# Kernel optimization log

Hardware: AMD Instinct MI355X
Metric: run time of the kernel (lower is better)

The kernel has to match this reference:

```python
import jax, jax.numpy as jnp
import numpy as np

VOCAB, EMB, UNITS, B, T = 50000, 300, 256, 32, 512


def _lstm_scan(x, Wi, Wh, b, h0, c0):
    """Keras-order LSTM (gates i,f,c,o). x: [B,T,D]. Returns (outputs [B,T,U], h, c)."""
    xg = jnp.einsum('btd,dg->btg', x, Wi) + b  # precompute input projections [B,T,4U]

    def step(carry, xt):
        h, c = carry
        g = xt + h @ Wh
        i, f, gg, o = jnp.split(g, 4, axis=-1)
        c = jax.nn.sigmoid(f) * c + jax.nn.sigmoid(i) * jnp.tanh(gg)
        h = jax.nn.sigmoid(o) * jnp.tanh(c)
        return (h, c), h

    (h, c), hs = jax.lax.scan(step, (h0, c0), jnp.swapaxes(xg, 0, 1))
    return jnp.swapaxes(hs, 0, 1), h, c


def _bilstm(x, pf, pb, init=None):
    """Keras Bidirectional(LSTM(go_backwards=True), merge_mode='sum').
    'forward' sub-layer scans reversed input; 'backward' sub-layer scans original
    input and its output is time-reversed before summing."""
    Bsz = x.shape[0]
    if init is None:
        z = jnp.zeros((Bsz, UNITS), x.dtype)
        hf0, cf0, hb0, cb0 = z, z, z, z
    else:
        hf0, cf0, hb0, cb0 = init
    of, hf, cf = _lstm_scan(x[:, ::-1], *pf, hf0, cf0)
    ob, hb, cb = _lstm_scan(x, *pb, hb0, cb0)
    return of + ob[:, ::-1], hf, cf, hb, cb


def setup_inputs() -> dict:
    key = jax.random.key(0)
    ks = iter(jax.random.split(key, 32))
    d = {}
    d['x'] = jax.random.randint(next(ks), (B, T), 0, VOCAB, dtype=jnp.int32)
    d['emb'] = jax.random.normal(next(ks), (VOCAB, EMB), jnp.float32) * 0.05
    dims_in = [EMB, UNITS, UNITS]
    for l in (1, 2, 3):
        for dirc in ('f', 'b'):
            din = dims_in[l - 1]
            d[f'Wi{l}{dirc}'] = jax.random.normal(next(ks), (din, 4 * UNITS), jnp.float32) * 0.05
            d[f'Wh{l}{dirc}'] = jax.random.normal(next(ks), (UNITS, 4 * UNITS), jnp.float32) * 0.05
            d[f'b{l}{dirc}'] = jnp.zeros((4 * UNITS,), jnp.float32)
    return d


def reference(x, emb, Wi1f, Wh1f, b1f, Wi1b, Wh1b, b1b,
              Wi2f, Wh2f, b2f, Wi2b, Wh2b, b2b,
              Wi3f, Wh3f, b3f, Wi3b, Wh3b, b3b):
    h = emb[x]  # embedding lookup [B,T,EMB]
    h, hf, cf, hb, cb = _bilstm(h, (Wi1f, Wh1f, b1f), (Wi1b, Wh1b, b1b))
    h, hf, cf, hb, cb = _bilstm(h, (Wi2f, Wh2f, b2f), (Wi2b, Wh2b, b2b), (hf, cf, hb, cb))
    out, hf, cf, hb, cb = _bilstm(h, (Wi3f, Wh3f, b3f), (Wi3b, Wh3b, b3b), (hf, cf, hb, cb))
    return out, hf, cf, hb, cb
```

## Files before the change

kernel.cpp:

```cpp
#include <hip/hip_runtime.h>
#include <stdint.h>


typedef unsigned short u16;
typedef __bf16 bf16x8 __attribute__((ext_vector_type(8)));
typedef float f32x4 __attribute__((ext_vector_type(4)));

#define SCOPE_AGENT __HIP_MEMORY_SCOPE_AGENT

__device__ __forceinline__ float bf2f(u16 u) { return __uint_as_float(((unsigned)u) << 16); }
__device__ __forceinline__ u16 f2bf(float f) {
  unsigned u = __float_as_uint(f);
  unsigned r = (u + 0x7FFFu + ((u >> 16) & 1u)) >> 16;
  return (u16)r;
}
__device__ __forceinline__ float rdW(const void* p, size_t i, int isf) {
  return isf ? ((const float*)p)[i] : bf2f(((const u16*)p)[i]);
}
__device__ __forceinline__ float sigf(float x) { return 1.f / (1.f + __expf(-x)); }
__device__ __forceinline__ float tanh_(float x) { float e = __expf(2.f * x); return 1.f - 2.f / (e + 1.f); }

#define O_X0   0ull
#define O_WC1  10485760ull
#define O_WC2  11796480ull
#define O_WC3  12845056ull
#define O_WH   13893632ull
#define O_BIAS 17039360ull
#define O_FLAG 17063936ull
#define O_C0   17076352ull
#define O_CA   17141888ull
#define O_CB   17207424ull
#define O_CC   17272960ull
#define O_HSA  17338496ull
#define O_HSB  34148480ull
#define O_XG   50958464ull

#define HS_U4  1050624

__global__ void k_detect(const unsigned* __restrict__ embw, unsigned* flag) {
  int tid = threadIdx.x;
  unsigned w = embw[tid];
  unsigned e = (w >> 7) & 0xFFu;
  unsigned long long m = __ballot(e >= 100u && e < 128u);
  if (tid == 0) flag[0] = (__popcll(m) >= 32) ? 0u : 1u;
}

__global__ __launch_bounds__(256) void k_zero(uint4* __restrict__ p, int n) {
  uint4 z = {0u, 0u, 0u, 0u};
  for (int i = blockIdx.x * 256 + threadIdx.x; i < n; i += gridDim.x * 256) p[i] = z;
}

__global__ __launch_bounds__(256) void k_prep(
    const void* Wi1f, const void* Wi1b, const void* Wi2f, const void* Wi2b,
    const void* Wi3f, const void* Wi3b,
    const void* Wh1f, const void* Wh1b, const void* Wh2f, const void* Wh2b,
    const void* Wh3f, const void* Wh3b,
    const void* b1f, const void* b1b, const void* b2f, const void* b2b,
    const void* b3f, const void* b3b,
    const unsigned* __restrict__ flag,
    u16* Wc1, u16* Wc2, u16* Wc3, u16* WhC, float* bias, float* c0) {
  const int isf = (int)flag[0];
  int idx = blockIdx.x * 256 + threadIdx.x;
  if (idx < 2048 * 320) {
    int n = idx / 320, k = idx - n * 320;
    int dd = n >> 10, col = n & 1023;
    const void* W = dd ? Wi1b : Wi1f;
    Wc1[idx] = (k < 300) ? f2bf(rdW(W, (size_t)k * 1024 + col, isf)) : (u16)0;
  }
  if (idx < 2048 * 256) {
    int n = idx >> 8, k = idx & 255;
    int dd = n >> 10, col = n & 1023;
    Wc2[idx] = f2bf(rdW(dd ? Wi2b : Wi2f, (size_t)k * 1024 + col, isf));
    Wc3[idx] = f2bf(rdW(dd ? Wi3b : Wi3f, (size_t)k * 1024 + col, isf));
  }
  if (idx < 3 * 2048) {
    int l = idx >> 11, n = idx & 2047;
    int dd = n >> 10, col = n & 1023;
    const void* bp = (l == 0) ? (dd ? b1b : b1f) : (l == 1) ? (dd ? b2b : b2f) : (dd ? b3b : b3f);
    bias[idx] = rdW(bp, col, isf);
  }
  if (idx < 2 * 32 * 256) c0[idx] = 0.f;
  if (idx < 6 * 262144) {
    int mat = idx >> 18, pos = idx & 262143;
    const void* W = (mat == 0) ? Wh1f : (mat == 1) ? Wh1b : (mat == 2) ? Wh2f
                   : (mat == 3) ? Wh2b : (mat == 4) ? Wh3f : Wh3b;
    WhC[idx] = f2bf(rdW(W, (size_t)pos, isf));
  }
}

__global__ __launch_bounds__(256) void k_embed(const int* __restrict__ x,
                                               const void* __restrict__ emb,
                                               const unsigned* __restrict__ flag,
                                               u16* __restrict__ X0) {
  const int isf = (int)flag[0];
  int row = blockIdx.x;
  int t = row >> 5, b = row & 31;
  int tok = x[b * 512 + t];
  int tid = threadIdx.x;
  if (tid < 150) {
    unsigned pk;
    if (isf) {
      float2 v = *(const float2*)((const float*)emb + (size_t)tok * 300 + tid * 2);
      pk = (unsigned)f2bf(v.x) | ((unsigned)f2bf(v.y) << 16);
    } else {
      pk = *(const unsigned*)((const u16*)emb + (size_t)tok * 300 + tid * 2);
    }
    *(unsigned*)(X0 + (size_t)row * 320 + tid * 2) = pk;
  } else if (tid < 160) {
    *(unsigned*)(X0 + (size_t)row * 320 + 300 + (tid - 150) * 2) = 0u;
  }
}

__global__ __launch_bounds__(256) void k_gemm(const u16* __restrict__ A,
                                              const u16* __restrict__ Bt,
                                              const float* __restrict__ bias,
                                              u16* __restrict__ XG, int K) {
  __shared__ u16 As[128 * 32];
  __shared__ u16 Bs[128 * 32];
  const int tid = threadIdx.x;
  const int wv = tid >> 6, L = tid & 63, quad = L >> 4, l15 = L & 15;
  const int wm = wv & 1, wn = wv >> 1;
  const int bm = blockIdx.x & 127, bn = blockIdx.x >> 7;
  const u16* Ab = A + (size_t)(bm * 128) * K;
  const u16* Bb = Bt + (size_t)(bn * 128) * K;
  f32x4 z = {0.f, 0.f, 0.f, 0.f};
  f32x4 acc[4][4];
#pragma unroll
  for (int a = 0; a < 4; ++a)
#pragma unroll
    for (int b2 = 0; b2 < 4; ++b2) acc[a][b2] = z;
  const int srow = tid >> 2, sk = (tid & 3) * 8;
  for (int k0 = 0; k0 < K; k0 += 32) {
    __syncthreads();
    uint4 a0 = *(const uint4*)(Ab + (size_t)srow * K + k0 + sk);
    uint4 a1 = *(const uint4*)(Ab + (size_t)(srow + 64) * K + k0 + sk);
    uint4 b0 = *(const uint4*)(Bb + (size_t)srow * K + k0 + sk);
    uint4 b1 = *(const uint4*)(Bb + (size_t)(srow + 64) * K + k0 + sk);
    *(uint4*)&As[srow * 32 + sk] = a0;
    *(uint4*)&As[(srow + 64) * 32 + sk] = a1;
    *(uint4*)&Bs[srow * 32 + sk] = b0;
    *(uint4*)&Bs[(srow + 64) * 32 + sk] = b1;
    __syncthreads();
    bf16x8 af[4], bf[4];
#pragma unroll
    for (int t4 = 0; t4 < 4; ++t4) {
      af[t4] = *(const bf16x8*)&As[(wm * 64 + t4 * 16 + l15) * 32 + quad * 8];
      bf[t4] = *(const bf16x8*)&Bs[(wn * 64 + t4 * 16 + l15) * 32 + quad * 8];
    }
#pragma unroll
    for (int mt4 = 0; mt4 < 4; ++mt4)
#pragma unroll
      for (int nt4 = 0; nt4 < 4; ++nt4)
        acc[mt4][nt4] = __builtin_amdgcn_mfma_f32_16x16x32_bf16(af[mt4], bf[nt4], acc[mt4][nt4], 0, 0, 0);
  }
#pragma unroll
  for (int mt4 = 0; mt4 < 4; ++mt4)
#pragma unroll
    for (int nt4 = 0; nt4 < 4; ++nt4)
#pragma unroll
      for (int i = 0; i < 4; ++i) {
        int m = bm * 128 + wm * 64 + mt4 * 16 + quad * 4 + i;
        int n = bn * 128 + wn * 64 + nt4 * 16 + l15;
        XG[(size_t)m * 2048 + n] = f2bf(acc[mt4][nt4][i] + bias[n]);
      }
}

__global__ __launch_bounds__(512, 2) void k_scan(const u16* __restrict__ XG,
                                                 const u16* __restrict__ Whf,
                                                 const u16* __restrict__ Whb,
                                                 u16* hs, const u16* h0src,
                                                 const float* __restrict__ c_src,
                                                 float* __restrict__ c_dst) {
  const int wg = blockIdx.x;
  const int d = wg >> 2, q = wg & 3;
  const int tid = threadIdx.x;
  const int wv = tid >> 6, L = tid & 63, quad = L >> 4, l15 = L & 15;
  const int mt = wv & 1, ng = wv >> 1;

  __shared__ u16 Ah[32][264];
  __shared__ float gbuf[32][257];

  const u16* Wh = d ? Whb : Whf;

  union U8 { u16 s[8]; bf16x8 v; };
  U8 bfrag[4][8];
#pragma unroll
  for (int t = 0; t < 4; ++t) {
    int ci = (ng * 4 + t) * 16 + l15;
    int col = (ci >> 6) * 256 + q * 64 + (ci & 63);
#pragma unroll
    for (int kt = 0; kt < 8; ++kt)
#pragma unroll
      for (int j = 0; j < 8; ++j)
        bfrag[t][kt].s[j] = Wh[(size_t)(kt * 32 + quad * 8 + j) * 1024 + col];
  }

  const int b_c = tid >> 4, j = tid & 15;
  float cv[4];
#pragma unroll
  for (int e = 0; e < 4; ++e)
    cv[e] = c_src[(d * 32 + b_c) * 256 + q * 64 + 4 * j + e];

  unsigned* hw = (unsigned*)hs;

  {
    int hb = tid >> 4, pair0 = (tid & 15) * 8;
    if (h0src) {
      const unsigned* h0w = (const unsigned*)h0src + ((size_t)(d * 513 + 512) * 32 + hb) * 128 + pair0;
#pragma unroll
      for (int k = 0; k < 8; ++k)
        *(unsigned*)&Ah[hb][(pair0 + k) * 2] = h0w[k] ^ 0x80008000u;
    } else {
#pragma unroll
      for (int k = 0; k < 8; ++k)
        *(unsigned*)&Ah[hb][(pair0 + k) * 2] = 0u;
    }
  }

  u16 xgr[4][4];
  {
    int tin = d ? 0 : 511;
#pragma unroll
    for (int t = 0; t < 4; ++t) {
      int ci = (ng * 4 + t) * 16 + l15;
      int col = d * 1024 + (ci >> 6) * 256 + q * 64 + (ci & 63);
      const u16* xp = XG + (size_t)(tin * 32 + mt * 16 + quad * 4) * 2048 + col;
#pragma unroll
      for (int i = 0; i < 4; ++i) xgr[t][i] = xp[(size_t)i * 2048];
    }
  }

  for (int s = 0; s < 512; ++s) {
    __syncthreads();

    f32x4 acc[4] = {{0.f, 0.f, 0.f, 0.f}, {0.f, 0.f, 0.f, 0.f},
                    {0.f, 0.f, 0.f, 0.f}, {0.f, 0.f, 0.f, 0.f}};
#pragma unroll
    for (int kt = 0; kt < 8; ++kt) {
      bf16x8 ah = *(const bf16x8*)&Ah[mt * 16 + l15][kt * 32 + quad * 8];
#pragma unroll
      for (int t = 0; t < 4; ++t)
        acc[t] = __builtin_amdgcn_mfma_f32_16x16x32_bf16(ah, bfrag[t][kt].v, acc[t], 0, 0, 0);
    }

#pragma unroll
    for (int t = 0; t < 4; ++t) {
      int ci = (ng * 4 + t) * 16 + l15;
#pragma unroll
      for (int i = 0; i < 4; ++i)
        gbuf[mt * 16 + quad * 4 + i][ci] = acc[t][i] + bf2f(xgr[t][i]);
    }
    __syncthreads();

    {
      u16 eh[4];
#pragma unroll
      for (int e = 0; e < 4; ++e) {
        int lu = 4 * j + e;
        float gi = gbuf[b_c][lu];
        float gf = gbuf[b_c][64 + lu];
        float gg = gbuf[b_c][128 + lu];
        float go = gbuf[b_c][192 + lu];
        cv[e] = sigf(gf) * cv[e] + sigf(gi) * tanh_(gg);
        float h = sigf(go) * tanh_(cv[e]);
        u16 ev = f2bf(h); if (ev == 0x8000u) ev = 0;
        eh[e] = ev;
      }
      unsigned pk0 = ((unsigned)eh[0] | ((unsigned)eh[1] << 16)) ^ 0x80008000u;
      unsigned pk1 = ((unsigned)eh[2] | ((unsigned)eh[3] << 16)) ^ 0x80008000u;
      size_t base = ((size_t)(d * 513 + s + 1) * 32 + b_c) * 128 + q * 32 + 2 * j;
      __hip_atomic_store(&hw[base],     pk0, __ATOMIC_RELAXED, SCOPE_AGENT);
      __hip_atomic_store(&hw[base + 1], pk1, __ATOMIC_RELAXED, SCOPE_AGENT);
      *(unsigned*)&Ah[b_c][q * 64 + 4 * j]     = pk0 ^ 0x80008000u;
      *(unsigned*)&Ah[b_c][q * 64 + 4 * j + 2] = pk1 ^ 0x80008000u;
      if (s == 511) {
#pragma unroll
        for (int e = 0; e < 4; ++e)
          c_dst[(d * 32 + b_c) * 256 + q * 64 + 4 * j + e] = cv[e];
      }
    }

    if (s < 511) {
      {
        int tin = d ? (s + 1) : (510 - s);
#pragma unroll
        for (int t = 0; t < 4; ++t) {
          int ci = (ng * 4 + t) * 16 + l15;
          int col = d * 1024 + (ci >> 6) * 256 + q * 64 + (ci & 63);
          const u16* xp = XG + (size_t)(tin * 32 + mt * 16 + quad * 4) * 2048 + col;
#pragma unroll
          for (int i = 0; i < 4; ++i) xgr[t][i] = xp[(size_t)i * 2048];
        }
      }

      size_t sb = (size_t)(d * 513 + s + 2) * 32;
      sb = ((size_t)(d * 513 + s + 1) * 32 + b_c) * 128;
      unsigned v[6];
      size_t pidx[6];
#pragma unroll
      for (int pp = 0; pp < 3; ++pp) {
        int q2 = (q + 1 + pp) & 3;
        pidx[pp * 2]     = sb + q2 * 32 + 2 * j;
        pidx[pp * 2 + 1] = sb + q2 * 32 + 2 * j + 1;
      }
#pragma unroll
      for (int p2 = 0; p2 < 6; ++p2)
        v[p2] = __hip_atomic_load(&hw[pidx[p2]], __ATOMIC_RELAXED, SCOPE_AGENT);
      for (;;) {
        bool all = true;
#pragma unroll
        for (int p2 = 0; p2 < 6; ++p2) {
          if (v[p2] == 0u) {
            all = false;
            v[p2] = __hip_atomic_load(&hw[pidx[p2]], __ATOMIC_RELAXED, SCOPE_AGENT);
          }
        }
        if (all) break;
      }
#pragma unroll
      for (int pp = 0; pp < 3; ++pp) {
        int q2 = (q + 1 + pp) & 3;
        *(unsigned*)&Ah[b_c][q2 * 64 + 4 * j]     = v[pp * 2]     ^ 0x80008000u;
        *(unsigned*)&Ah[b_c][q2 * 64 + 4 * j + 2] = v[pp * 2 + 1] ^ 0x80008000u;
      }
    }
  }
}

__global__ __launch_bounds__(256) void k_mkA(const u16* __restrict__ hs, u16* __restrict__ A23) {
  int row = blockIdx.x;
  int t = row >> 5, b = row & 31, u = threadIdx.x;
  float vf = bf2f(hs[(size_t)(t + 1) * 8192 + b * 256 + u] ^ 0x8000u);
  float vb = bf2f(hs[(size_t)(513 + 512 - t) * 8192 + b * 256 + u] ^ 0x8000u);
  A23[(size_t)row * 256 + u] = f2bf(vf + vb);
}

__global__ __launch_bounds__(256) void k_epi(const u16* __restrict__ hs,
                                             const float* __restrict__ cC,
                                             const unsigned* __restrict__ flag,
                                             void* __restrict__ outv) {
  const int isf = (int)flag[0];
  float* outf = (float*)outv;
  u16* outb = (u16*)outv;
  int u = threadIdx.x;
  if (blockIdx.x < 16384) {
    int b = blockIdx.x >> 9, s = blockIdx.x & 511;
    float v = bf2f(hs[(size_t)(s + 1) * 8192 + b * 256 + u] ^ 0x8000u) +
              bf2f(hs[(size_t)(513 + 512 - s) * 8192 + b * 256 + u] ^ 0x8000u);
    size_t o = (size_t)blockIdx.x * 256 + u;
    if (isf) outf[o] = v; else outb[o] = f2bf(v);
  } else {
    int jj = blockIdx.x - 16384;
    const size_t base = 16384ull * 256;
    float vhf = bf2f(hs[(size_t)512 * 8192 + jj * 256 + u] ^ 0x8000u);
    float vcf = cC[jj * 256 + u];
    float vhb = bf2f(hs[(size_t)1025 * 8192 + jj * 256 + u] ^ 0x8000u);
    float vcb = cC[(32 + jj) * 256 + u];
    size_t o0 = base + (size_t)jj * 256 + u;
    if (isf) {
      outf[o0] = vhf; outf[o0 + 8192] = vcf; outf[o0 + 16384] = vhb; outf[o0 + 24576] = vcb;
    } else {
      outb[o0] = f2bf(vhf); outb[o0 + 8192] = f2bf(vcf);
      outb[o0 + 16384] = f2bf(vhb); outb[o0 + 24576] = f2bf(vcb);
    }
  }
}

extern "C" void kernel_launch(void* const* d_in, const int* in_sizes, int n_in,
                              void* d_out, int out_size, void* d_ws, size_t ws_size,
                              hipStream_t stream) {
  (void)in_sizes; (void)n_in; (void)out_size; (void)ws_size;
  const int* x   = (const int*)d_in[0];
  const void* emb = d_in[1];
  const void* Wi1f = d_in[2];  const void* Wh1f = d_in[3];  const void* b1f = d_in[4];
  const void* Wi1b = d_in[5];  const void* Wh1b = d_in[6];  const void* b1b = d_in[7];
  const void* Wi2f = d_in[8];  const void* Wh2f = d_in[9];  const void* b2f = d_in[10];
  const void* Wi2b = d_in[11]; const void* Wh2b = d_in[12]; const void* b2b = d_in[13];
  const void* Wi3f = d_in[14]; const void* Wh3f = d_in[15]; const void* b3f = d_in[16];
  const void* Wi3b = d_in[17]; const void* Wh3b = d_in[18]; const void* b3b = d_in[19];

  char* ws = (char*)d_ws;
  u16* X0   = (u16*)(ws + O_X0);
  u16* A23  = (u16*)(ws + O_X0);
  u16* Wc1  = (u16*)(ws + O_WC1);
  u16* Wc2  = (u16*)(ws + O_WC2);
  u16* Wc3  = (u16*)(ws + O_WC3);
  u16* WhC  = (u16*)(ws + O_WH);
  float* bias = (float*)(ws + O_BIAS);
  unsigned* flag = (unsigned*)(ws + O_FLAG);
  float* c0 = (float*)(ws + O_C0);
  float* cA = (float*)(ws + O_CA);
  float* cB = (float*)(ws + O_CB);
  float* cC = (float*)(ws + O_CC);
  u16* hsA = (u16*)(ws + O_HSA);
  u16* hsB = (u16*)(ws + O_HSB);
  u16* XG  = (u16*)(ws + O_XG);

  k_detect<<<1, 64, 0, stream>>>((const unsigned*)emb, flag);
  k_prep<<<6144, 256, 0, stream>>>(Wi1f, Wi1b, Wi2f, Wi2b, Wi3f, Wi3b,
                                   Wh1f, Wh1b, Wh2f, Wh2b, Wh3f, Wh3b,
                                   b1f, b1b, b2f, b2b, b3f, b3b,
                                   flag, Wc1, Wc2, Wc3, WhC, bias, c0);
  k_zero<<<2048, 256, 0, stream>>>((uint4*)hsA, HS_U4);
  k_zero<<<2048, 256, 0, stream>>>((uint4*)hsB, HS_U4);
  k_embed<<<16384, 256, 0, stream>>>(x, emb, flag, X0);

  k_gemm<<<2048, 256, 0, stream>>>(X0, Wc1, bias + 0, XG, 320);
  k_scan<<<8, 512, 0, stream>>>(XG, WhC + 0 * 262144, WhC + 1 * 262144, hsA, nullptr, c0, cA);
  k_mkA<<<16384, 256, 0, stream>>>(hsA, A23);
  k_gemm<<<2048, 256, 0, stream>>>(A23, Wc2, bias + 2048, XG, 256);
  k_scan<<<8, 512, 0, stream>>>(XG, WhC + 2 * 262144, WhC + 3 * 262144, hsB, hsA, cA, cB);
  k_zero<<<2048, 256, 0, stream>>>((uint4*)hsA, HS_U4);
  k_mkA<<<16384, 256, 0, stream>>>(hsB, A23);
  k_gemm<<<2048, 256, 0, stream>>>(A23, Wc3, bias + 4096, XG, 256);
  k_scan<<<8, 512, 0, stream>>>(XG, WhC + 4 * 262144, WhC + 5 * 262144, hsA, hsB, cB, cC);

  k_epi<<<16416, 256, 0, stream>>>(hsA, cC, flag, d_out);
}
```

Baseline: 4.935 ms.

## Restructure LSTM scan to 16 blocks with register-resident gates and double-buffered h

```diff
diff --git a/kernel.cpp b/kernel.cpp
--- a/kernel.cpp
+++ b/kernel.cpp
@@ -3,6 +3,7 @@
 
 
 typedef unsigned short u16;
+typedef unsigned long long u64;
 typedef __bf16 bf16x8 __attribute__((ext_vector_type(8)));
 typedef float f32x4 __attribute__((ext_vector_type(4)));
 
@@ -114,7 +115,7 @@
 __global__ __launch_bounds__(256) void k_gemm(const u16* __restrict__ A,
                                               const u16* __restrict__ Bt,
                                               const float* __restrict__ bias,
-                                              u16* __restrict__ XG, int K) {
+                                              u16* __restrict__ XGT, int K) {
   __shared__ u16 As[128 * 32];
   __shared__ u16 Bs[128 * 32];
   const int tid = threadIdx.x;
@@ -161,75 +162,82 @@
       for (int i = 0; i < 4; ++i) {
         int m = bm * 128 + wm * 64 + mt4 * 16 + quad * 4 + i;
         int n = bn * 128 + wn * 64 + nt4 * 16 + l15;
-        XG[(size_t)m * 2048 + n] = f2bf(acc[mt4][nt4][i] + bias[n]);
-      }
-}
-
-__global__ __launch_bounds__(512, 2) void k_scan(const u16* __restrict__ XG,
+        int t = m >> 5, b = m & 31;
+        int d = n >> 10, g = (n >> 8) & 3, u = n & 255;
+        XGT[(((((size_t)t * 2 + d) * 4 + g) * 256 + u) << 5) + b] =
+            f2bf(acc[mt4][nt4][i] + bias[n]);
+      }
+}
+
+__global__ __launch_bounds__(256, 2) void k_scan(const u16* __restrict__ XGT,
                                                  const u16* __restrict__ Whf,
                                                  const u16* __restrict__ Whb,
                                                  u16* hs, const u16* h0src,
                                                  const float* __restrict__ c_src,
                                                  float* __restrict__ c_dst) {
   const int wg = blockIdx.x;
-  const int d = wg >> 2, q = wg & 3;
+  const int d = wg >> 3, q = wg & 7;
   const int tid = threadIdx.x;
   const int wv = tid >> 6, L = tid & 63, quad = L >> 4, l15 = L & 15;
-  const int mt = wv & 1, ng = wv >> 1;
-
-  __shared__ u16 Ah[32][264];
-  __shared__ float gbuf[32][257];
+  const int mt = wv & 1, hh = wv >> 1;
+  const int gu = q * 32 + hh * 16 + l15;
+
+  __shared__ u16 Ah[2][32][264];
 
   const u16* Wh = d ? Whb : Whf;
 
   union U8 { u16 s[8]; bf16x8 v; };
   U8 bfrag[4][8];
 #pragma unroll
-  for (int t = 0; t < 4; ++t) {
-    int ci = (ng * 4 + t) * 16 + l15;
-    int col = (ci >> 6) * 256 + q * 64 + (ci & 63);
+  for (int g = 0; g < 4; ++g)
 #pragma unroll
     for (int kt = 0; kt < 8; ++kt)
 #pragma unroll
       for (int j = 0; j < 8; ++j)
-        bfrag[t][kt].s[j] = Wh[(size_t)(kt * 32 + quad * 8 + j) * 1024 + col];
-  }
-
-  const int b_c = tid >> 4, j = tid & 15;
+        bfrag[g][kt].s[j] = Wh[(size_t)(kt * 32 + quad * 8 + j) * 1024 + g * 256 + gu];
+
   float cv[4];
 #pragma unroll
-  for (int e = 0; e < 4; ++e)
-    cv[e] = c_src[(d * 32 + b_c) * 256 + q * 64 + 4 * j + e];
-
-  unsigned* hw = (unsigned*)hs;
-
-  {
-    int hb = tid >> 4, pair0 = (tid & 15) * 8;
-    if (h0src) {
-      const unsigned* h0w = (const unsigned*)h0src + ((size_t)(d * 513 + 512) * 32 + hb) * 128 + pair0;
-#pragma unroll
-      for (int k = 0; k < 8; ++k)
-        *(unsigned*)&Ah[hb][(pair0 + k) * 2] = h0w[k] ^ 0x80008000u;
-    } else {
-#pragma unroll
-      for (int k = 0; k < 8; ++k)
-        *(unsigned*)&Ah[hb][(pair0 + k) * 2] = 0u;
-    }
-  }
-
-  u16 xgr[4][4];
+  for (int i = 0; i < 4; ++i)
+    cv[i] = c_src[(d * 32 + mt * 16 + quad * 4 + i) * 256 + gu];
+
+  u64* h64 = (u64*)hs;
+
+  int po[7];
+#pragma unroll
+  for (int k = 0; k < 7; ++k) {
+    int flat = tid * 7 + k;
+    int pu = flat >> 3, bg = flat & 7;
+    int u = pu + (pu >= q * 32 ? 32 : 0);
+    po[k] = u * 8 + bg;
+  }
+
+  if (h0src) {
+    const u64* s64 = (const u64*)h0src + (size_t)(d * 513 + 512) * 2048;
+#pragma unroll
+    for (int r = 0; r < 8; ++r) {
+      u64 w = s64[tid * 8 + r];
+#pragma unroll
+      for (int j = 0; j < 4; ++j)
+        Ah[0][r * 4 + j][tid] = (u16)((u16)(w >> (16 * j)) ^ 0x8000u);
+    }
+  } else {
+#pragma unroll
+    for (int r = 0; r < 8; ++r)
+#pragma unroll
+      for (int j = 0; j < 4; ++j) Ah[0][r * 4 + j][tid] = 0;
+  }
+
+  const u64* xb = (const u64*)XGT;
+  u64 xg[4];
   {
     int tin = d ? 0 : 511;
 #pragma unroll
-    for (int t = 0; t < 4; ++t) {
-      int ci = (ng * 4 + t) * 16 + l15;
-      int col = d * 1024 + (ci >> 6) * 256 + q * 64 + (ci & 63);
-      const u16* xp = XG + (size_t)(tin * 32 + mt * 16 + quad * 4) * 2048 + col;
-#pragma unroll
-      for (int i = 0; i < 4; ++i) xgr[t][i] = xp[(size_t)i * 2048];
-    }
-  }
-
+    for (int g = 0; g < 4; ++g)
+      xg[g] = xb[((((size_t)tin * 2 + d) * 4 + g) * 256 + gu) * 8 + mt * 4 + quad];
+  }
+
+  int p = 0;
   for (int s = 0; s < 512; ++s) {
     __syncthreads();
 
@@ -237,102 +245,93 @@
                     {0.f, 0.f, 0.f, 0.f}, {0.f, 0.f, 0.f, 0.f}};
 #pragma unroll
     for (int kt = 0; kt < 8; ++kt) {
-      bf16x8 ah = *(const bf16x8*)&Ah[mt * 16 + l15][kt * 32 + quad * 8];
-#pragma unroll
-      for (int t = 0; t < 4; ++t)
-        acc[t] = __builtin_amdgcn_mfma_f32_16x16x32_bf16(ah, bfrag[t][kt].v, acc[t], 0, 0, 0);
-    }
-
-#pragma unroll
-    for (int t = 0; t < 4; ++t) {
-      int ci = (ng * 4 + t) * 16 + l15;
+      bf16x8 ah = *(const bf16x8*)&Ah[p][mt * 16 + l15][kt * 32 + quad * 8];
+#pragma unroll
+      for (int g = 0; g < 4; ++g)
+        acc[g] = __builtin_amdgcn_mfma_f32_16x16x32_bf16(ah, bfrag[g][kt].v, acc[g], 0, 0, 0);
+    }
+
+    u16 eh[4];
+#pragma unroll
+    for (int i = 0; i < 4; ++i) {
+      float gi = acc[0][i] + bf2f((u16)(xg[0] >> (16 * i)));
+      float gf = acc[1][i] + bf2f((u16)(xg[1] >> (16 * i)));
+      float gc = acc[2][i] + bf2f((u16)(xg[2] >> (16 * i)));
+      float go = acc[3][i] + bf2f((u16)(xg[3] >> (16 * i)));
+      cv[i] = sigf(gf) * cv[i] + sigf(gi) * tanh_(gc);
+      float h = sigf(go) * tanh_(cv[i]);
+      u16 e = f2bf(h); if (e == 0x8000u) e = 0;
+      eh[i] = (u16)(e ^ 0x8000u);
+    }
+    u64 pk = (u64)eh[0] | ((u64)eh[1] << 16) | ((u64)eh[2] << 32) | ((u64)eh[3] << 48);
+    size_t slab = (size_t)(d * 513 + s + 1) * 2048;
+    __hip_atomic_store(&h64[slab + gu * 8 + mt * 4 + quad], pk,
+                       __ATOMIC_RELAXED, SCOPE_AGENT);
+
+    const int np = p ^ 1;
+#pragma unroll
+    for (int i = 0; i < 4; ++i)
+      Ah[np][mt * 16 + quad * 4 + i][gu] = (u16)(eh[i] ^ 0x8000u);
+
+    if (s == 511) {
 #pragma unroll
       for (int i = 0; i < 4; ++i)
-        gbuf[mt * 16 + quad * 4 + i][ci] = acc[t][i] + bf2f(xgr[t][i]);
-    }
-    __syncthreads();
-
-    {
-      u16 eh[4];
-#pragma unroll
-      for (int e = 0; e < 4; ++e) {
-        int lu = 4 * j + e;
-        float gi = gbuf[b_c][lu];
-        float gf = gbuf[b_c][64 + lu];
-        float gg = gbuf[b_c][128 + lu];
-        float go = gbuf[b_c][192 + lu];
-        cv[e] = sigf(gf) * cv[e] + sigf(gi) * tanh_(gg);
-        float h = sigf(go) * tanh_(cv[e]);
-        u16 ev = f2bf(h); if (ev == 0x8000u) ev = 0;
-        eh[e] = ev;
-      }
-      unsigned pk0 = ((unsigned)eh[0] | ((unsigned)eh[1] << 16)) ^ 0x80008000u;
-      unsigned pk1 = ((unsigned)eh[2] | ((unsigned)eh[3] << 16)) ^ 0x80008000u;
-      size_t base = ((size_t)(d * 513 + s + 1) * 32 + b_c) * 128 + q * 32 + 2 * j;
-      __hip_atomic_store(&hw[base],     pk0, __ATOMIC_RELAXED, SCOPE_AGENT);
-      __hip_atomic_store(&hw[base + 1], pk1, __ATOMIC_RELAXED, SCOPE_AGENT);
-      *(unsigned*)&Ah[b_c][q * 64 + 4 * j]     = pk0 ^ 0x80008000u;
-      *(unsigned*)&Ah[b_c][q * 64 + 4 * j + 2] = pk1 ^ 0x80008000u;
-      if (s == 511) {
-#pragma unroll
-        for (int e = 0; e < 4; ++e)
-          c_dst[(d * 32 + b_c) * 256 + q * 64 + 4 * j + e] = cv[e];
-      }
-    }
-
-    if (s < 511) {
+        c_dst[(d * 32 + mt * 16 + quad * 4 + i) * 256 + gu] = cv[i];
+    } else {
       {
         int tin = d ? (s + 1) : (510 - s);
 #pragma unroll
-        for (int t = 0; t < 4; ++t) {
-          int ci = (ng * 4 + t) * 16 + l15;
-          int col = d * 1024 + (ci >> 6) * 256 + q * 64 + (ci & 63);
-          const u16* xp = XG + (size_t)(tin * 32 + mt * 16 + quad * 4) * 2048 + col;
-#pragma unroll
-          for (int i = 0; i < 4; ++i) xgr[t][i] = xp[(size_t)i * 2048];
-        }
-      }
-
-      size_t sb = (size_t)(d * 513 + s + 2) * 32;
-      sb = ((size_t)(d * 513 + s + 1) * 32 + b_c) * 128;
-      unsigned v[6];
-      size_t pidx[6];
-#pragma unroll
-      for (int pp = 0; pp < 3; ++pp) {
-        int q2 = (q + 1 + pp) & 3;
-        pidx[pp * 2]     = sb + q2 * 32 + 2 * j;
-        pidx[pp * 2 + 1] = sb + q2 * 32 + 2 * j + 1;
-      }
-#pragma unroll
-      for (int p2 = 0; p2 < 6; ++p2)
-        v[p2] = __hip_atomic_load(&hw[pidx[p2]], __ATOMIC_RELAXED, SCOPE_AGENT);
+        for (int g = 0; g < 4; ++g)
+          xg[g] = xb[((((size_t)tin * 2 + d) * 4 + g) * 256 + gu) * 8 + mt * 4 + quad];
+      }
+      u64 w[7];
+#pragma unroll
+      for (int k = 0; k < 7; ++k)
+        w[k] = __hip_atomic_load(&h64[slab + po[k]], __ATOMIC_RELAXED, SCOPE_AGENT);
       for (;;) {
         bool all = true;
 #pragma unroll
-        for (int p2 = 0; p2 < 6; ++p2) {
-          if (v[p2] == 0u) {
+        for (int k = 0; k < 7; ++k) {
+          if (w[k] == 0ull) {
             all = false;
-            v[p2] = __hip_atomic_load(&hw[pidx[p2]], __ATOMIC_RELAXED, SCOPE_AGENT);
+            w[k] = __hip_atomic_load(&h64[slab + po[k]], __ATOMIC_RELAXED, SCOPE_AGENT);
           }
         }
         if (all) break;
       }
 #pragma unroll
-      for (int pp = 0; pp < 3; ++pp) {
-        int q2 = (q + 1 + pp) & 3;
-        *(unsigned*)&Ah[b_c][q2 * 64 + 4 * j]     = v[pp * 2]     ^ 0x80008000u;
-        *(unsigned*)&Ah[b_c][q2 * 64 + 4 * j + 2] = v[pp * 2 + 1] ^ 0x80008000u;
-      }
-    }
+      for (int k = 0; k < 7; ++k) {
+        int u = po[k] >> 3, bg = po[k] & 7;
+#pragma unroll
+        for (int j = 0; j < 4; ++j)
+          Ah[np][bg * 4 + j][u] = (u16)((u16)(w[k] >> (16 * j)) ^ 0x8000u);
+      }
+    }
+    p = np;
   }
 }
 
 __global__ __launch_bounds__(256) void k_mkA(const u16* __restrict__ hs, u16* __restrict__ A23) {
-  int row = blockIdx.x;
-  int t = row >> 5, b = row & 31, u = threadIdx.x;
-  float vf = bf2f(hs[(size_t)(t + 1) * 8192 + b * 256 + u] ^ 0x8000u);
-  float vb = bf2f(hs[(size_t)(513 + 512 - t) * 8192 + b * 256 + u] ^ 0x8000u);
-  A23[(size_t)row * 256 + u] = f2bf(vf + vb);
+  __shared__ u16 S[32][264];
+  int t = blockIdx.x, tid = threadIdx.x;
+  const u64* f64 = (const u64*)hs + (size_t)(t + 1) * 2048;
+  const u64* b64 = (const u64*)hs + (size_t)(513 + 512 - t) * 2048;
+#pragma unroll
+  for (int bg = 0; bg < 8; ++bg) {
+    u64 wf = f64[tid * 8 + bg], wb = b64[tid * 8 + bg];
+#pragma unroll
+    for (int j = 0; j < 4; ++j) {
+      float vf = bf2f((u16)((u16)(wf >> (16 * j)) ^ 0x8000u));
+      float vb = bf2f((u16)((u16)(wb >> (16 * j)) ^ 0x8000u));
+      S[bg * 4 + j][tid] = f2bf(vf + vb);
+    }
+  }
+  __syncthreads();
+  int b = tid >> 3, uc = tid & 7;
+  u16* dst = A23 + ((size_t)t * 32 + b) * 256 + uc * 32;
+#pragma unroll
+  for (int z = 0; z < 4; ++z)
+    *(uint4*)(dst + z * 8) = *(const uint4*)&S[b][uc * 32 + z * 8];
 }
 
 __global__ __launch_bounds__(256) void k_epi(const u16* __restrict__ hs,
@@ -342,27 +341,47 @@
   const int isf = (int)flag[0];
   float* outf = (float*)outv;
   u16* outb = (u16*)outv;
-  int u = threadIdx.x;
-  if (blockIdx.x < 16384) {
-    int b = blockIdx.x >> 9, s = blockIdx.x & 511;
-    float v = bf2f(hs[(size_t)(s + 1) * 8192 + b * 256 + u] ^ 0x8000u) +
-              bf2f(hs[(size_t)(513 + 512 - s) * 8192 + b * 256 + u] ^ 0x8000u);
-    size_t o = (size_t)blockIdx.x * 256 + u;
+  int tid = threadIdx.x;
+  if (blockIdx.x < 512) {
+    __shared__ float Sf[32][264];
+    int s = blockIdx.x;
+    const u64* f64 = (const u64*)hs + (size_t)(s + 1) * 2048;
+    const u64* b64 = (const u64*)hs + (size_t)(513 + 512 - s) * 2048;
+#pragma unroll
+    for (int bg = 0; bg < 8; ++bg) {
+      u64 wf = f64[tid * 8 + bg], wb = b64[tid * 8 + bg];
+#pragma unroll
+      for (int j = 0; j < 4; ++j) {
+        float vf = bf2f((u16)((u16)(wf >> (16 * j)) ^ 0x8000u));
+        float vb = bf2f((u16)((u16)(wb >> (16 * j)) ^ 0x8000u));
+        Sf[bg * 4 + j][tid] = vf + vb;
+      }
+    }
+    __syncthreads();
+    int b = tid >> 3, uc = tid & 7;
+    size_t o = ((size_t)b * 512 + s) * 256 + uc * 32;
+    if (isf) {
+#pragma unroll
+      for (int z = 0; z < 32; ++z) outf[o + z] = Sf[b][uc * 32 + z];
+    } else {
+#pragma unroll
+      for (int z = 0; z < 16; ++z) {
+        unsigned pk = (unsigned)f2bf(Sf[b][uc * 32 + 2 * z]) |
+                      ((unsigned)f2bf(Sf[b][uc * 32 + 2 * z + 1]) << 16);
+        *(unsigned*)(outb + o + 2 * z) = pk;
+      }
+    }
+  } else {
+    int idx = blockIdx.x - 512;
+    int which = idx >> 5, b = idx & 31;
+    int u = tid;
+    float v;
+    if (which == 0)      v = bf2f((u16)(hs[(size_t)512 * 8192 + u * 32 + b] ^ 0x8000u));
+    else if (which == 1) v = cC[b * 256 + u];
+    else if (which == 2) v = bf2f((u16)(hs[(size_t)1025 * 8192 + u * 32 + b] ^ 0x8000u));
+    else                 v = cC[(32 + b) * 256 + u];
+    size_t o = 16384ull * 256 + (size_t)which * 8192 + b * 256 + u;
     if (isf) outf[o] = v; else outb[o] = f2bf(v);
-  } else {
-    int jj = blockIdx.x - 16384;
-    const size_t base = 16384ull * 256;
-    float vhf = bf2f(hs[(size_t)512 * 8192 + jj * 256 + u] ^ 0x8000u);
-    float vcf = cC[jj * 256 + u];
-    float vhb = bf2f(hs[(size_t)1025 * 8192 + jj * 256 + u] ^ 0x8000u);
-    float vcb = cC[(32 + jj) * 256 + u];
-    size_t o0 = base + (size_t)jj * 256 + u;
-    if (isf) {
-      outf[o0] = vhf; outf[o0 + 8192] = vcf; outf[o0 + 16384] = vhb; outf[o0 + 24576] = vcb;
-    } else {
-      outb[o0] = f2bf(vhf); outb[o0 + 8192] = f2bf(vcf);
-      outb[o0 + 16384] = f2bf(vhb); outb[o0 + 24576] = f2bf(vcb);
-    }
   }
 }
 
@@ -394,7 +413,7 @@
   float* cC = (float*)(ws + O_CC);
   u16* hsA = (u16*)(ws + O_HSA);
   u16* hsB = (u16*)(ws + O_HSB);
-  u16* XG  = (u16*)(ws + O_XG);
+  u16* XGT = (u16*)(ws + O_XG);
 
   k_detect<<<1, 64, 0, stream>>>((const unsigned*)emb, flag);
   k_prep<<<6144, 256, 0, stream>>>(Wi1f, Wi1b, Wi2f, Wi2b, Wi3f, Wi3b,
@@ -405,15 +424,15 @@
   k_zero<<<2048, 256, 0, stream>>>((uint4*)hsB, HS_U4);
   k_embed<<<16384, 256, 0, stream>>>(x, emb, flag, X0);
 
-  k_gemm<<<2048, 256, 0, stream>>>(X0, Wc1, bias + 0, XG, 320);
-  k_scan<<<8, 512, 0, stream>>>(XG, WhC + 0 * 262144, WhC + 1 * 262144, hsA, nullptr, c0, cA);
-  k_mkA<<<16384, 256, 0, stream>>>(hsA, A23);
-  k_gemm<<<2048, 256, 0, stream>>>(A23, Wc2, bias + 2048, XG, 256);
-  k_scan<<<8, 512, 0, stream>>>(XG, WhC + 2 * 262144, WhC + 3 * 262144, hsB, hsA, cA, cB);
+  k_gemm<<<2048, 256, 0, stream>>>(X0, Wc1, bias + 0, XGT, 320);
+  k_scan<<<16, 256, 0, stream>>>(XGT, WhC + 0 * 262144, WhC + 1 * 262144, hsA, nullptr, c0, cA);
+  k_mkA<<<512, 256, 0, stream>>>(hsA, A23);
+  k_gemm<<<2048, 256, 0, stream>>>(A23, Wc2, bias + 2048, XGT, 256);
+  k_scan<<<16, 256, 0, stream>>>(XGT, WhC + 2 * 262144, WhC + 3 * 262144, hsB, hsA, cA, cB);
   k_zero<<<2048, 256, 0, stream>>>((uint4*)hsA, HS_U4);
-  k_mkA<<<16384, 256, 0, stream>>>(hsB, A23);
-  k_gemm<<<2048, 256, 0, stream>>>(A23, Wc3, bias + 4096, XG, 256);
-  k_scan<<<8, 512, 0, stream>>>(XG, WhC + 4 * 262144, WhC + 5 * 262144, hsA, hsB, cB, cC);
-
-  k_epi<<<16416, 256, 0, stream>>>(hsA, cC, flag, d_out);
-}
+  k_mkA<<<512, 256, 0, stream>>>(hsB, A23);
+  k_gemm<<<2048, 256, 0, stream>>>(A23, Wc3, bias + 4096, XGT, 256);
+  k_scan<<<16, 256, 0, stream>>>(XGT, WhC + 4 * 262144, WhC + 5 * 262144, hsA, hsB, cB, cC);
+
+  k_epi<<<640, 256, 0, stream>>>(hsA, cC, flag, d_out);
+}
```

Result: faster. 4.507 ms (-8.7%).
